# Performance work log

Hardware: AMD Instinct MI355X
Metric: run time of the kernel (lower is better)

The kernel has to match this reference:

```python
import jax, jax.numpy as jnp
import numpy as np


def setup_inputs() -> dict:
    key = jax.random.key(0)
    k1, k2, k3, k4 = jax.random.split(key, 4)
    B, T, D = 32, 2048, 128
    queries = jax.random.normal(k1, (B, T, D), dtype=jnp.float32)
    keys = jax.random.normal(k2, (B, T, D), dtype=jnp.float32)
    values = jax.random.normal(k3, (B, T, D), dtype=jnp.float32)
    valid_lens = jax.random.randint(k4, (B,), 0, T, dtype=jnp.int32)
    return {"queries": queries, "keys": keys, "values": values, "valid_lens": valid_lens}


def reference(queries, keys, values, valid_lens):
    d = queries.shape[-1]
    scale = d / 0.5  # faithful to source: 2*d, NOT sqrt(d)
    # (B, Tq, Tk) scores
    scores = jnp.einsum('bqd,bkd->bqk', queries, keys) / scale
    T = scores.shape[-1]
    # lengths (B,) -> mask (B, 1, Tk), broadcast over query rows
    mask = jnp.arange(T) < valid_lens[:, None, None]
    neg_inf = jnp.finfo(scores.dtype).min
    logits = jnp.where(mask, scores, neg_inf)
    probs = jax.nn.softmax(logits, axis=-1)
    fully_masked = ~jnp.any(mask, axis=-1, keepdims=True)
    probs = jnp.where(fully_masked, jnp.zeros_like(probs), probs)
    # dropout p=0.0 -> identity
    return jnp.einsum('bqk,bkv->bqv', probs, values)
```

## Files before the change

kernel.cpp:

```cpp
#include <hip/hip_runtime.h>
#include <hip/hip_bf16.h>

#define B_ 32
#define T_ 2048
#define D_ 128
#define BQ 64
#define BK 64

typedef __attribute__((ext_vector_type(8))) __bf16 bf16x8;
typedef __attribute__((ext_vector_type(16))) float f32x16;

__device__ __forceinline__ float fast_exp2(float x) {
#if __has_builtin(__builtin_amdgcn_exp2f)
    return __builtin_amdgcn_exp2f(x);
#else
    return exp2f(x);
#endif
}

__device__ __forceinline__ f32x16 zero16() {
    f32x16 z;
    #pragma unroll
    for (int i = 0; i < 16; ++i) z[i] = 0.f;
    return z;
}

__global__ __launch_bounds__(256, 4)
void prep_k(const float* __restrict__ K, const int* __restrict__ vlens,
            __hip_bfloat16* __restrict__ Kb)
{
    const int b = blockIdx.y, k0 = blockIdx.x * 64;
    const int kmax = (vlens[b] + 63) & ~63;
    if (k0 >= kmax) return;
    const float4* src = (const float4*)(K + ((size_t)b * T_ + k0) * D_);
    uint2* dst = (uint2*)(Kb + ((size_t)b * T_ + k0) * D_);
    #pragma unroll
    for (int it = 0; it < 8; ++it) {
        int c = it * 256 + threadIdx.x;
        float4 v = src[c];
        union { __hip_bfloat16 h[4]; uint2 u; } pk;
        pk.h[0] = __float2bfloat16(v.x); pk.h[1] = __float2bfloat16(v.y);
        pk.h[2] = __float2bfloat16(v.z); pk.h[3] = __float2bfloat16(v.w);
        dst[c] = pk.u;
    }
}

__global__ __launch_bounds__(256, 2)
void prep_vt(const float* __restrict__ V, const int* __restrict__ vlens,
             __hip_bfloat16* __restrict__ VTb)
{
    __shared__ float tile[64][132];
    const int b = blockIdx.y, k0 = blockIdx.x * 64;
    const int kmax = (vlens[b] + 63) & ~63;
    if (k0 >= kmax) return;
    const float4* src = (const float4*)(V + ((size_t)b * T_ + k0) * D_);
    #pragma unroll
    for (int it = 0; it < 8; ++it) {
        int c = it * 256 + threadIdx.x;
        int row = c >> 5, c4 = c & 31;
        *(float4*)&tile[row][c4 * 4] = src[c];
    }
    __syncthreads();
    #pragma unroll
    for (int it = 0; it < 8; ++it) {
        int c = it * 256 + threadIdx.x;
        int kc = c & 15, d = c >> 4;
        union { __hip_bfloat16 h[4]; uint2 u; } pk;
        #pragma unroll
        for (int j = 0; j < 4; ++j) {
            int jj = (j + kc) & 3;
            pk.h[jj] = __float2bfloat16(tile[kc * 4 + jj][d]);
        }
        *(uint2*)(VTb + ((size_t)b * D_ + d) * T_ + k0 + kc * 4) = pk.u;
    }
}

__global__ __launch_bounds__(128, 2)
void attn_main(const float* __restrict__ Q, const int* __restrict__ vlens,
               const __hip_bfloat16* __restrict__ Kb,
               const __hip_bfloat16* __restrict__ VTb,
               float* __restrict__ out)
{
    const int tid  = threadIdx.x;
    const int wave = tid >> 6;
    const int lane = tid & 63;
    const int l32  = lane & 31;
    const int hi   = lane >> 5;

    const int b    = blockIdx.y;
    const int q0   = blockIdx.x * BQ;
    const int vlen = vlens[b];
    const int nkb  = (vlen + 63) >> 6;

    __shared__ __hip_bfloat16 sK [64][136];
    __shared__ __hip_bfloat16 sVT[128][72];
    __shared__ __hip_bfloat16 sP [64][72];

    bf16x8 qf[8];
    {
        const float* qp = Q + ((size_t)b * T_ + q0 + wave * 32 + l32) * D_ + hi * 8;
        #pragma unroll
        for (int ds = 0; ds < 8; ++ds) {
            const float4* p4 = (const float4*)(qp + ds * 16);
            float4 a = p4[0], c = p4[1];
            __hip_bfloat16 h[8] = {
                __float2bfloat16(a.x), __float2bfloat16(a.y),
                __float2bfloat16(a.z), __float2bfloat16(a.w),
                __float2bfloat16(c.x), __float2bfloat16(c.y),
                __float2bfloat16(c.z), __float2bfloat16(c.w) };
            qf[ds] = *(const bf16x8*)h;
        }
    }

    bf16x8 ones;
    #pragma unroll
    for (int j = 0; j < 8; ++j) ones[j] = (__bf16)1.0f;

    f32x16 o[4];
    #pragma unroll
    for (int dt = 0; dt < 4; ++dt) o[dt] = zero16();
    f32x16 lacc = zero16();

    const float C = 1.4426950408889634f / 256.0f;

    for (int kb = 0; kb < nkb; ++kb) {
        const int k0 = kb * 64;
        __syncthreads();

        {
            const __hip_bfloat16* kbase = Kb + ((size_t)b * T_ + k0) * D_;
            #pragma unroll
            for (int it = 0; it < 8; ++it) {
                int c = it * 128 + tid;
                int row = c >> 4, cc = c & 15;
                uint4 v = *(const uint4*)(kbase + row * D_ + cc * 8);
                *(uint4*)&sK[row][cc * 8] = v;
            }
            const __hip_bfloat16* vbase = VTb + (size_t)b * D_ * T_ + k0;
            #pragma unroll
            for (int it = 0; it < 8; ++it) {
                int c = it * 128 + tid;
                int d = c >> 3, cc = c & 7;
                uint4 v = *(const uint4*)(vbase + (size_t)d * T_ + cc * 8);
                *(uint4*)&sVT[d][cc * 8] = v;
            }
        }
        __syncthreads();

        f32x16 s[2];
        s[0] = zero16(); s[1] = zero16();
        #pragma unroll
        for (int nt = 0; nt < 2; ++nt)
            #pragma unroll
            for (int ds = 0; ds < 8; ++ds) {
                bf16x8 kf = *(const bf16x8*)&sK[nt * 32 + l32][ds * 16 + hi * 8];
                s[nt] = __builtin_amdgcn_mfma_f32_32x32x16_bf16(qf[ds], kf, s[nt], 0, 0, 0);
            }

        #pragma unroll
        for (int nt = 0; nt < 2; ++nt) {
            const bool valid = (k0 + nt * 32 + l32) < vlen;
            #pragma unroll
            for (int r = 0; r < 16; ++r) {
                float e = fast_exp2(s[nt][r] * C);
                e = valid ? e : 0.f;
                int q = (r & 3) + 8 * (r >> 2) + 4 * hi + wave * 32;
                sP[q][nt * 32 + l32] = __float2bfloat16(e);
            }
        }

        #pragma unroll
        for (int ks = 0; ks < 4; ++ks) {
            bf16x8 pf = *(const bf16x8*)&sP[wave * 32 + l32][ks * 16 + hi * 8];
            lacc = __builtin_amdgcn_mfma_f32_32x32x16_bf16(pf, ones, lacc, 0, 0, 0);
            #pragma unroll
            for (int dt = 0; dt < 4; ++dt) {
                bf16x8 vf = *(const bf16x8*)&sVT[dt * 32 + l32][ks * 16 + hi * 8];
                o[dt] = __builtin_amdgcn_mfma_f32_32x32x16_bf16(pf, vf, o[dt], 0, 0, 0);
            }
        }
    }

    float inv[16];
    #pragma unroll
    for (int r = 0; r < 16; ++r) inv[r] = (lacc[r] > 0.f) ? 1.0f / lacc[r] : 0.f;
    #pragma unroll
    for (int dt = 0; dt < 4; ++dt)
        #pragma unroll
        for (int r = 0; r < 16; ++r) {
            int q = (r & 3) + 8 * (r >> 2) + 4 * hi + wave * 32;
            out[((size_t)b * T_ + q0 + q) * D_ + dt * 32 + l32] = o[dt][r] * inv[r];
        }
}

extern "C" void kernel_launch(void* const* d_in, const int* in_sizes, int n_in,
                              void* d_out, int out_size, void* d_ws, size_t ws_size,
                              hipStream_t stream) {
    const float* Q = (const float*)d_in[0];
    const float* K = (const float*)d_in[1];
    const float* V = (const float*)d_in[2];
    const int* vl  = (const int*)d_in[3];
    float* out     = (float*)d_out;

    const size_t kb_bytes = (size_t)B_ * T_ * D_ * 2;
    if (ws_size < 2 * kb_bytes) return;
    __hip_bfloat16* Kb  = (__hip_bfloat16*)d_ws;
    __hip_bfloat16* VTb = (__hip_bfloat16*)((char*)d_ws + kb_bytes);

    prep_k <<<dim3(T_ / 64, B_), 256, 0, stream>>>(K, vl, Kb);
    prep_vt<<<dim3(T_ / 64, B_), 256, 0, stream>>>(V, vl, VTb);
    attn_main<<<dim3(T_ / BQ, B_), 128, 0, stream>>>(Q, vl, Kb, VTb, out);
}
```

Baseline: 225.4 us.

## Prefetch next K/V tile into registers, fuse prep kernels, swap grid order

The main attention loop now issues global loads for the next K and V^T tile into registers while the current tile is being computed, which hides global-memory latency behind the MFMA work. The K conversion and V transpose prep kernels are merged into a single launch to save one kernel launch. The grid axes are swapped so consecutive blocks belong to different batches, which changes scheduling order and load balance across uneven valid lengths. The cost is 64 extra VGPRs per thread for the prefetch buffers, which may hurt occupancy or cause spills.

```diff
diff --git a/kernel.cpp b/kernel.cpp
--- a/kernel.cpp
+++ b/kernel.cpp
@@ -5,7 +5,6 @@
 #define T_ 2048
 #define D_ 128
 #define BQ 64
-#define BK 64
 
 typedef __attribute__((ext_vector_type(8))) __bf16 bf16x8;
 typedef __attribute__((ext_vector_type(16))) float f32x16;
@@ -25,53 +24,50 @@
     return z;
 }
 
-__global__ __launch_bounds__(256, 4)
-void prep_k(const float* __restrict__ K, const int* __restrict__ vlens,
-            __hip_bfloat16* __restrict__ Kb)
-{
-    const int b = blockIdx.y, k0 = blockIdx.x * 64;
-    const int kmax = (vlens[b] + 63) & ~63;
-    if (k0 >= kmax) return;
-    const float4* src = (const float4*)(K + ((size_t)b * T_ + k0) * D_);
-    uint2* dst = (uint2*)(Kb + ((size_t)b * T_ + k0) * D_);
-    #pragma unroll
-    for (int it = 0; it < 8; ++it) {
-        int c = it * 256 + threadIdx.x;
-        float4 v = src[c];
-        union { __hip_bfloat16 h[4]; uint2 u; } pk;
-        pk.h[0] = __float2bfloat16(v.x); pk.h[1] = __float2bfloat16(v.y);
-        pk.h[2] = __float2bfloat16(v.z); pk.h[3] = __float2bfloat16(v.w);
-        dst[c] = pk.u;
-    }
-}
-
 __global__ __launch_bounds__(256, 2)
-void prep_vt(const float* __restrict__ V, const int* __restrict__ vlens,
-             __hip_bfloat16* __restrict__ VTb)
+void prep(const float* __restrict__ K, const float* __restrict__ V,
+          const int* __restrict__ vlens,
+          __hip_bfloat16* __restrict__ Kb, __hip_bfloat16* __restrict__ VTb)
 {
     __shared__ float tile[64][132];
     const int b = blockIdx.y, k0 = blockIdx.x * 64;
     const int kmax = (vlens[b] + 63) & ~63;
     if (k0 >= kmax) return;
-    const float4* src = (const float4*)(V + ((size_t)b * T_ + k0) * D_);
-    #pragma unroll
-    for (int it = 0; it < 8; ++it) {
-        int c = it * 256 + threadIdx.x;
-        int row = c >> 5, c4 = c & 31;
-        *(float4*)&tile[row][c4 * 4] = src[c];
-    }
-    __syncthreads();
-    #pragma unroll
-    for (int it = 0; it < 8; ++it) {
-        int c = it * 256 + threadIdx.x;
-        int kc = c & 15, d = c >> 4;
-        union { __hip_bfloat16 h[4]; uint2 u; } pk;
-        #pragma unroll
-        for (int j = 0; j < 4; ++j) {
-            int jj = (j + kc) & 3;
-            pk.h[jj] = __float2bfloat16(tile[kc * 4 + jj][d]);
-        }
-        *(uint2*)(VTb + ((size_t)b * D_ + d) * T_ + k0 + kc * 4) = pk.u;
+
+    {
+        const float4* src = (const float4*)(K + ((size_t)b * T_ + k0) * D_);
+        uint2* dst = (uint2*)(Kb + ((size_t)b * T_ + k0) * D_);
+        #pragma unroll
+        for (int it = 0; it < 8; ++it) {
+            int c = it * 256 + threadIdx.x;
+            float4 v = src[c];
+            union { __hip_bfloat16 h[4]; uint2 u; } pk;
+            pk.h[0] = __float2bfloat16(v.x); pk.h[1] = __float2bfloat16(v.y);
+            pk.h[2] = __float2bfloat16(v.z); pk.h[3] = __float2bfloat16(v.w);
+            dst[c] = pk.u;
+        }
+    }
+    {
+        const float4* src = (const float4*)(V + ((size_t)b * T_ + k0) * D_);
+        #pragma unroll
+        for (int it = 0; it < 8; ++it) {
+            int c = it * 256 + threadIdx.x;
+            int row = c >> 5, c4 = c & 31;
+            *(float4*)&tile[row][c4 * 4] = src[c];
+        }
+        __syncthreads();
+        #pragma unroll
+        for (int it = 0; it < 8; ++it) {
+            int c = it * 256 + threadIdx.x;
+            int kc = c & 15, d = c >> 4;
+            union { __hip_bfloat16 h[4]; uint2 u; } pk;
+            #pragma unroll
+            for (int j = 0; j < 4; ++j) {
+                int jj = (j + kc) & 3;
+                pk.h[jj] = __float2bfloat16(tile[kc * 4 + jj][d]);
+            }
+            *(uint2*)(VTb + ((size_t)b * D_ + d) * T_ + k0 + kc * 4) = pk.u;
+        }
     }
 }
 
@@ -87,8 +83,8 @@
     const int l32  = lane & 31;
     const int hi   = lane >> 5;
 
-    const int b    = blockIdx.y;
-    const int q0   = blockIdx.x * BQ;
+    const int b    = blockIdx.x;
+    const int q0   = blockIdx.y * BQ;
     const int vlen = vlens[b];
     const int nkb  = (vlen + 63) >> 6;
 
@@ -123,28 +119,47 @@
 
     const float C = 1.4426950408889634f / 256.0f;
 
+    const __hip_bfloat16* kb_base = Kb + (size_t)b * T_ * D_;
+    const __hip_bfloat16* vt_base = VTb + (size_t)b * D_ * T_;
+
+    uint4 kpf[8], vpf[8];
+    #define ISSUE(KB)                                                          \
+        do {                                                                   \
+            const __hip_bfloat16* kbp = kb_base + (size_t)(KB) * 64 * D_;      \
+            _Pragma("unroll")                                                  \
+            for (int it = 0; it < 8; ++it) {                                   \
+                int c = it * 128 + tid;                                        \
+                int row = c >> 4, cc = c & 15;                                 \
+                kpf[it] = *(const uint4*)(kbp + row * D_ + cc * 8);            \
+            }                                                                  \
+            const __hip_bfloat16* vbp = vt_base + (KB) * 64;                   \
+            _Pragma("unroll")                                                  \
+            for (int it = 0; it < 8; ++it) {                                   \
+                int c = it * 128 + tid;                                        \
+                int d = c >> 3, cc = c & 7;                                    \
+                vpf[it] = *(const uint4*)(vbp + (size_t)d * T_ + cc * 8);      \
+            }                                                                  \
+        } while (0)
+
+    if (nkb > 0) ISSUE(0);
+
     for (int kb = 0; kb < nkb; ++kb) {
         const int k0 = kb * 64;
         __syncthreads();
 
-        {
-            const __hip_bfloat16* kbase = Kb + ((size_t)b * T_ + k0) * D_;
-            #pragma unroll
-            for (int it = 0; it < 8; ++it) {
-                int c = it * 128 + tid;
-                int row = c >> 4, cc = c & 15;
-                uint4 v = *(const uint4*)(kbase + row * D_ + cc * 8);
-                *(uint4*)&sK[row][cc * 8] = v;
-            }
-            const __hip_bfloat16* vbase = VTb + (size_t)b * D_ * T_ + k0;
-            #pragma unroll
-            for (int it = 0; it < 8; ++it) {
-                int c = it * 128 + tid;
-                int d = c >> 3, cc = c & 7;
-                uint4 v = *(const uint4*)(vbase + (size_t)d * T_ + cc * 8);
-                *(uint4*)&sVT[d][cc * 8] = v;
-            }
-        }
+        #pragma unroll
+        for (int it = 0; it < 8; ++it) {
+            int c = it * 128 + tid;
+            int row = c >> 4, cc = c & 15;
+            *(uint4*)&sK[row][cc * 8] = kpf[it];
+        }
+        #pragma unroll
+        for (int it = 0; it < 8; ++it) {
+            int c = it * 128 + tid;
+            int d = c >> 3, cc = c & 7;
+            *(uint4*)&sVT[d][cc * 8] = vpf[it];
+        }
+        if (kb + 1 < nkb) ISSUE(kb + 1);
         __syncthreads();
 
         f32x16 s[2];
@@ -180,6 +195,7 @@
             }
         }
     }
+    #undef ISSUE
 
     float inv[16];
     #pragma unroll
@@ -207,7 +223,6 @@
     __hip_bfloat16* Kb  = (__hip_bfloat16*)d_ws;
     __hip_bfloat16* VTb = (__hip_bfloat16*)((char*)d_ws + kb_bytes);
 
-    prep_k <<<dim3(T_ / 64, B_), 256, 0, stream>>>(K, vl, Kb);
-    prep_vt<<<dim3(T_ / 64, B_), 256, 0, stream>>>(V, vl, VTb);
-    attn_main<<<dim3(T_ / BQ, B_), 128, 0, stream>>>(Q, vl, Kb, VTb, out);
-}
+    prep<<<dim3(T_ / 64, B_), 256, 0, stream>>>(K, V, vl, Kb, VTb);
+    attn_main<<<dim3(B_, T_ / BQ), 128, 0, stream>>>(Q, vl, Kb, VTb, out);
+}
```

After: 438.4 us. 94.5% more time.
